# Kernel optimization log

Measured on AMD Instinct MI355X. Metric: run time of the kernel, lower is better.

The kernel has to match this reference:

```python
import jax, jax.numpy as jnp
import numpy as np

B, C, H, W = 4, 256, 64, 64
CR = max(C // 8, 1)  # reduced channels
EPS = 1e-12  # F.normalize eps


def setup_inputs() -> dict:
    key = jax.random.key(0)
    ks = jax.random.split(key, 8)
    s = 1.0 / np.sqrt(C)
    return {
        "x": jax.random.normal(ks[0], (B, C, H, W), dtype=jnp.float32),
        "Wq": jax.random.normal(ks[1], (CR, C), dtype=jnp.float32) * s,
        "bq": jax.random.normal(ks[2], (CR,), dtype=jnp.float32) * s,
        "Wk": jax.random.normal(ks[3], (CR, C), dtype=jnp.float32) * s,
        "bk": jax.random.normal(ks[4], (CR,), dtype=jnp.float32) * s,
        "Wv": jax.random.normal(ks[5], (C, C), dtype=jnp.float32) * s,
        "bv": jax.random.normal(ks[6], (C,), dtype=jnp.float32) * s,
        "gamma": jax.random.normal(ks[7], (1,), dtype=jnp.float32),
    }


def reference(x, Wq, bq, Wk, bk, Wv, bv, gamma):
    b, c, h, w = x.shape
    xf = x.reshape(b, c, h * w)  # [B, C, N]
    # 1x1 convs are per-pixel linear maps
    q = jnp.einsum("rc,bcn->brn", Wq, xf) + bq[None, :, None]  # [B, CR, N]
    k = jnp.einsum("rc,bcn->brn", Wk, xf) + bk[None, :, None]  # [B, CR, N]
    v = jnp.einsum("dc,bcn->bdn", Wv, xf) + bv[None, :, None]  # [B, C, N]
    # attention = bmm(key^T, query): [B, N, N]
    attn = jnp.einsum("brn,brm->bnm", k, q)
    attn = jax.nn.relu(attn)
    # L1 normalize along dim=1 (rows), matching F.normalize(p=1, dim=1)
    denom = jnp.maximum(jnp.sum(jnp.abs(attn), axis=1, keepdims=True), EPS)
    attn = attn / denom
    out = jnp.einsum("bcn,bnm->bcm", v, attn).reshape(b, c, h, w)
    return gamma[0] * out + x
```

## Files before the change

### kernel.cpp

```cpp
#include <hip/hip_runtime.h>
#include <hip/hip_bf16.h>

#define NB 4
#define NC 256
#define NN 4096
#define NCR 32
#define PITCH 72

typedef __attribute__((ext_vector_type(8))) short short8_t;
typedef __attribute__((ext_vector_type(4))) float f32x4;
typedef __attribute__((ext_vector_type(2))) int int2_t;
typedef __attribute__((ext_vector_type(4))) int int4_t;
typedef __attribute__((ext_vector_type(4))) float float4_t;

static __device__ __forceinline__ unsigned short f2bf(float f) {
  unsigned u = __builtin_bit_cast(unsigned, f);
  u += 0x7FFFu + ((u >> 16) & 1u);
  return (unsigned short)(u >> 16);
}

static __device__ __forceinline__ unsigned cvt_pk(float lo, float hi) {
  unsigned r;
  asm("v_cvt_pk_bf16_f32 %0, %1, %2" : "=v"(r) : "v"(lo), "v"(hi));
  return r;
}

static __device__ __forceinline__ void lds_barrier() {
  asm volatile("s_waitcnt lgkmcnt(0)\n\ts_barrier" ::: "memory");
}

__global__ __launch_bounds__(64) void pack_w_kernel(
    const float* __restrict__ Wq, const float* __restrict__ Wk,
    const float* __restrict__ Wv, unsigned short* __restrict__ Wbf)
{
  const int row = blockIdx.x;
  const int t = threadIdx.x;
  const float* src = row < 32 ? Wq + (size_t)row * NC
                   : (row < 64 ? Wk + (size_t)(row - 32) * NC
                               : Wv + (size_t)(row - 64) * NC);
  float4_t v = *(const float4_t*)(src + t * 4);
  int2_t p;
  p[0] = cvt_pk(v[0], v[1]);
  p[1] = cvt_pk(v[2], v[3]);
  *(int2_t*)(Wbf + (size_t)row * NC + t * 4) = p;
}

__global__ __launch_bounds__(256) void xpose_kernel(
    const float* __restrict__ x, unsigned short* __restrict__ xT)
{
  __shared__ float tile[32][65];
  const int bid = blockIdx.x;
  const int mt = bid & 63, kt = (bid >> 6) & 7, b = bid >> 9;
  const int m0 = mt * 64, k0 = kt * 32;
  const int tid = threadIdx.x;

  const float* xb = x + (size_t)b * NC * NN + (size_t)k0 * NN + m0;
#pragma unroll
  for (int p = 0; p < 8; p++) {
    const int r = p * 4 + (tid >> 6);
    tile[r][tid & 63] = xb[(size_t)r * NN + (tid & 63)];
  }
  __syncthreads();

  const int m = tid >> 2, kq = (tid & 3) * 8;
  int4_t o;
#pragma unroll
  for (int j = 0; j < 4; j++)
    o[j] = cvt_pk(tile[kq + 2 * j][m], tile[kq + 2 * j + 1][m]);
  *(int4_t*)(xT + ((size_t)b * NN + m0 + m) * NC + k0 + kq) = o;
}

__global__ __launch_bounds__(256, 2) void qkv_kernel(
    const unsigned short* __restrict__ xT, const unsigned short* __restrict__ Wbf,
    const float* __restrict__ bq, const float* __restrict__ bk,
    const float* __restrict__ bv,
    unsigned short* __restrict__ Qt, unsigned short* __restrict__ Kt,
    unsigned short* __restrict__ Vt)
{
  const int bid = blockIdx.x;
  const int b   = bid >> 7;
  const int m0  = (bid & 127) * 32;
  const int tid = threadIdx.x;
  const int w    = tid >> 6;
  const int lane = tid & 63;
  const int lg   = lane >> 4;
  const int lm   = lane & 15;

  const unsigned short* xrow0 = xT + ((size_t)b * NN + m0 + lm) * NC + lg * 8;
  const unsigned short* xrow1 = xrow0 + 16 * NC;
  const unsigned short* wrow  = Wbf + (size_t)(w * 80 + lm) * NC + lg * 8;

  const f32x4 zero4 = {0.f, 0.f, 0.f, 0.f};
  f32x4 acc[5][2];
#pragma unroll
  for (int df = 0; df < 5; df++)
#pragma unroll
    for (int mf = 0; mf < 2; mf++) acc[df][mf] = zero4;

#pragma unroll
  for (int kc = 0; kc < 8; kc++) {
    const short8_t xf0 = *(const short8_t*)(xrow0 + kc * 32);
    const short8_t xf1 = *(const short8_t*)(xrow1 + kc * 32);
#pragma unroll
    for (int df = 0; df < 5; df++) {
      const short8_t wf = *(const short8_t*)(wrow + (size_t)df * 16 * NC + kc * 32);
      acc[df][0] = __builtin_amdgcn_mfma_f32_16x16x32_bf16(xf0, wf, acc[df][0], 0, 0, 0);
      acc[df][1] = __builtin_amdgcn_mfma_f32_16x16x32_bf16(xf1, wf, acc[df][1], 0, 0, 0);
    }
  }

#pragma unroll
  for (int df = 0; df < 5; df++) {
    const int dbase = w * 80 + df * 16;
    if (dbase < 64) {
      const bool isq = dbase < 32;
      const float bia = isq ? bq[dbase + lm] : bk[dbase - 32 + lm];
      unsigned short* dst = isq ? Qt : Kt;
      const int dcol = (isq ? dbase : dbase - 32) + lm;
#pragma unroll
      for (int mf = 0; mf < 2; mf++)
#pragma unroll
        for (int i = 0; i < 4; i++) {
          const int m = m0 + mf * 16 + lg * 4 + i;
          dst[((size_t)b * NN + m) * NCR + dcol] = f2bf(acc[df][mf][i] + bia);
        }
    } else {
      const int c = dbase - 64 + lm;
      const float bia = bv[c];
#pragma unroll
      for (int mf = 0; mf < 2; mf++) {
        int2_t p;
        p[0] = cvt_pk(acc[df][mf][0] + bia, acc[df][mf][1] + bia);
        p[1] = cvt_pk(acc[df][mf][2] + bia, acc[df][mf][3] + bia);
        *(int2_t*)(Vt + ((size_t)b * NC + c) * NN + m0 + mf * 16 + lg * 4) = p;
      }
    }
  }
}

__global__ __launch_bounds__(256, 2) void attn_kernel(
    const unsigned short* __restrict__ Qt, const unsigned short* __restrict__ Kt,
    const unsigned short* __restrict__ Vt, const float* __restrict__ x,
    const float* __restrict__ gamma, float* __restrict__ out)
{
  __shared__ unsigned short Slds[2][64 * PITCH];
  __shared__ float dlds[4][64];

  const int bid = blockIdx.x;
  const int xcd = bid & 7;
  const int b   = xcd >> 1;
  const int ch  = xcd & 1;
  const int m0  = (bid >> 3) * 64;
  const int tid = threadIdx.x;
  const int w    = tid >> 6;
  const int lane = tid & 63;
  const int lg   = lane >> 4;
  const int lm   = lane & 15;

  const unsigned short* Qb = Qt + (size_t)b * NN * NCR;
  const unsigned short* Kp = Kt + (size_t)b * NN * NCR +
                             (size_t)(w * 16 + lm) * NCR + lg * 8;
  const unsigned short* pV[2];
#pragma unroll
  for (int cf = 0; cf < 2; cf++)
    pV[cf] = Vt + ((size_t)b * NC + ch * 128 + w * 32 + cf * 16 + lm) * NN + lg * 8;

  short8_t qf[4];
#pragma unroll
  for (int mf = 0; mf < 4; mf++)
    qf[mf] = *(const short8_t*)(Qb + (size_t)(m0 + mf * 16 + lm) * NCR + lg * 8);

  const f32x4 zero4 = {0.f, 0.f, 0.f, 0.f};
  f32x4 acc[2][4];
#pragma unroll
  for (int cf = 0; cf < 2; cf++)
#pragma unroll
    for (int mf = 0; mf < 4; mf++) acc[cf][mf] = zero4;
  float dsum[4] = {0.f, 0.f, 0.f, 0.f};

  short8_t kA, kB, vA[2][2], vB[2][2];
  kA = *(const short8_t*)(Kp);
#pragma unroll
  for (int cf = 0; cf < 2; cf++) {
    vA[cf][0] = *(const short8_t*)(pV[cf]);
    vA[cf][1] = *(const short8_t*)(pV[cf] + 32);
  }

  const int swofs = w * 16 + lg * 4;

#define AITER(T, KC, KN, VC, VN, BUF) {                                       \
    const int n1 = (((T) + 1) & 63) * 64;                                     \
        \
    KN = *(const short8_t*)(Kp + (size_t)n1 * NCR);                           \
    _Pragma("unroll") for (int cf = 0; cf < 2; cf++) {                        \
      VN[cf][0] = *(const short8_t*)(pV[cf] + n1);                            \
      VN[cf][1] = *(const short8_t*)(pV[cf] + n1 + 32);                       \
    }                                                                         \
    _Pragma("unroll") for (int mf = 0; mf < 4; mf++) {                        \
      f32x4 s = __builtin_amdgcn_mfma_f32_16x16x32_bf16(KC, qf[mf], zero4, 0, 0, 0); \
      float s0 = fmaxf(s[0], 0.f), s1 = fmaxf(s[1], 0.f);                     \
      float s2 = fmaxf(s[2], 0.f), s3 = fmaxf(s[3], 0.f);                     \
      dsum[mf] += (s0 + s1) + (s2 + s3);                                      \
      int2_t p; p[0] = cvt_pk(s0, s1); p[1] = cvt_pk(s2, s3);                 \
      *(int2_t*)(&Slds[BUF][(mf * 16 + lm) * PITCH + swofs]) = p;             \
    }                                                                         \
    lds_barrier();                                                            \
    __builtin_amdgcn_s_setprio(1);                                            \
    _Pragma("unroll") for (int nch = 0; nch < 2; nch++) {                     \
      short8_t sf[4];                                                         \
      _Pragma("unroll") for (int mf = 0; mf < 4; mf++)                        \
        sf[mf] = *(const short8_t*)(&Slds[BUF][(mf * 16 + lm) * PITCH +       \
                                              nch * 32 + lg * 8]);            \
      _Pragma("unroll") for (int cf = 0; cf < 2; cf++)                        \
        _Pragma("unroll") for (int mf = 0; mf < 4; mf++)                      \
          acc[cf][mf] = __builtin_amdgcn_mfma_f32_16x16x32_bf16(              \
              VC[cf][nch], sf[mf], acc[cf][mf], 0, 0, 0);                     \
    }                                                                         \
    __builtin_amdgcn_s_setprio(0);                                            \
  }

#pragma unroll 1
  for (int t = 0; t < 64; t += 2) {
    AITER(t, kA, kB, vA, vB, 0)
    AITER(t + 1, kB, kA, vB, vA, 1)
  }
#undef AITER

#pragma unroll
  for (int mf = 0; mf < 4; mf++) {
    float v = dsum[mf];
    v += __shfl_xor(v, 16);
    v += __shfl_xor(v, 32);
    if (lane < 16) dlds[w][mf * 16 + lane] = v;
  }
  __syncthreads();

  const float g0 = gamma[0];
  float rden[4];
#pragma unroll
  for (int mf = 0; mf < 4; mf++) {
    const int mloc = mf * 16 + lm;
    float den = dlds[0][mloc] + dlds[1][mloc] + dlds[2][mloc] + dlds[3][mloc];
    den = den > 1e-12f ? den : 1e-12f;
    rden[mf] = 1.0f / den;
  }

  const float* xb = x + (size_t)b * NC * NN;
  float* ob = out + (size_t)b * NC * NN;
#pragma unroll
  for (int cf = 0; cf < 2; cf++) {
#pragma unroll
    for (int i = 0; i < 4; i++) {
      const int c = ch * 128 + w * 32 + cf * 16 + lg * 4 + i;
#pragma unroll
      for (int mf = 0; mf < 4; mf++) {
        const int m = m0 + mf * 16 + lm;
        ob[(size_t)c * NN + m] = g0 * acc[cf][mf][i] * rden[mf] + xb[(size_t)c * NN + m];
      }
    }
  }
}

extern "C" void kernel_launch(void* const* d_in, const int* in_sizes, int n_in,
                              void* d_out, int out_size, void* d_ws, size_t ws_size,
                              hipStream_t stream) {
  const float* x     = (const float*)d_in[0];
  const float* Wq    = (const float*)d_in[1];
  const float* bq    = (const float*)d_in[2];
  const float* Wk    = (const float*)d_in[3];
  const float* bk    = (const float*)d_in[4];
  const float* Wv    = (const float*)d_in[5];
  const float* bv    = (const float*)d_in[6];
  const float* gamma = (const float*)d_in[7];
  float* out = (float*)d_out;

  unsigned short* Wbf = (unsigned short*)d_ws;
  unsigned short* xT  = Wbf + (size_t)320 * NC;
  unsigned short* Qt  = xT + (size_t)NB * NN * NC;
  unsigned short* Kt  = Qt + (size_t)NB * NN * NCR;
  unsigned short* Vt  = Kt + (size_t)NB * NN * NCR;

  hipLaunchKernelGGL(pack_w_kernel, dim3(320), dim3(64), 0, stream,
                     Wq, Wk, Wv, Wbf);
  hipLaunchKernelGGL(xpose_kernel, dim3(2048), dim3(256), 0, stream, x, xT);
  hipLaunchKernelGGL(qkv_kernel, dim3(512), dim3(256), 0, stream,
                     xT, Wbf, bq, bk, bv, Qt, Kt, Vt);
  hipLaunchKernelGGL(attn_kernel, dim3(512), dim3(256), 0, stream,
                     Qt, Kt, Vt, x, gamma, out);
}
```

Before: 102.3 us.

## Fuse x transpose into QKV kernel and software-pipeline attention S computation

Drops the separate transpose kernel. The QKV kernel now reads fp32 x directly, converts it to bf16 and stages it in a swizzled shared-memory tile, double-buffered across four K chunks. This removes a kernel launch and the round trip of the bf16 xT buffer through global memory. In the attention kernel, the score MFMA for the next tile is computed while the current tile's PV accumulation runs, with K prefetched two tiles ahead. This trades extra registers and a restructured barrier schedule for more overlap between the two stages.

```diff
diff --git a/kernel.cpp b/kernel.cpp
--- a/kernel.cpp
+++ b/kernel.cpp
@@ -45,38 +45,15 @@
   *(int2_t*)(Wbf + (size_t)row * NC + t * 4) = p;
 }
 
-__global__ __launch_bounds__(256) void xpose_kernel(
-    const float* __restrict__ x, unsigned short* __restrict__ xT)
-{
-  __shared__ float tile[32][65];
-  const int bid = blockIdx.x;
-  const int mt = bid & 63, kt = (bid >> 6) & 7, b = bid >> 9;
-  const int m0 = mt * 64, k0 = kt * 32;
-  const int tid = threadIdx.x;
-
-  const float* xb = x + (size_t)b * NC * NN + (size_t)k0 * NN + m0;
-#pragma unroll
-  for (int p = 0; p < 8; p++) {
-    const int r = p * 4 + (tid >> 6);
-    tile[r][tid & 63] = xb[(size_t)r * NN + (tid & 63)];
-  }
-  __syncthreads();
-
-  const int m = tid >> 2, kq = (tid & 3) * 8;
-  int4_t o;
-#pragma unroll
-  for (int j = 0; j < 4; j++)
-    o[j] = cvt_pk(tile[kq + 2 * j][m], tile[kq + 2 * j + 1][m]);
-  *(int4_t*)(xT + ((size_t)b * NN + m0 + m) * NC + k0 + kq) = o;
-}
-
 __global__ __launch_bounds__(256, 2) void qkv_kernel(
-    const unsigned short* __restrict__ xT, const unsigned short* __restrict__ Wbf,
+    const float* __restrict__ x, const unsigned short* __restrict__ Wbf,
     const float* __restrict__ bq, const float* __restrict__ bk,
     const float* __restrict__ bv,
     unsigned short* __restrict__ Qt, unsigned short* __restrict__ Kt,
     unsigned short* __restrict__ Vt)
 {
+  __shared__ unsigned short xT[2][32 * 64];
+
   const int bid = blockIdx.x;
   const int b   = bid >> 7;
   const int m0  = (bid & 127) * 32;
@@ -86,9 +63,10 @@
   const int lg   = lane >> 4;
   const int lm   = lane & 15;
 
-  const unsigned short* xrow0 = xT + ((size_t)b * NN + m0 + lm) * NC + lg * 8;
-  const unsigned short* xrow1 = xrow0 + 16 * NC;
-  const unsigned short* wrow  = Wbf + (size_t)(w * 80 + lm) * NC + lg * 8;
+  const int mcol = tid & 31, kg = tid >> 5;
+  const float* xld = x + (size_t)b * NC * NN + (size_t)(kg * 8) * NN + m0 + mcol;
+  const int wofs = mcol * 64 + ((kg ^ (mcol & 7)) << 3);
+  const unsigned short* wrow = Wbf + (size_t)(w * 80 + lm) * NC;
 
   const f32x4 zero4 = {0.f, 0.f, 0.f, 0.f};
   f32x4 acc[5][2];
@@ -97,17 +75,42 @@
 #pragma unroll
     for (int mf = 0; mf < 2; mf++) acc[df][mf] = zero4;
 
-#pragma unroll
-  for (int kc = 0; kc < 8; kc++) {
-    const short8_t xf0 = *(const short8_t*)(xrow0 + kc * 32);
-    const short8_t xf1 = *(const short8_t*)(xrow1 + kc * 32);
-#pragma unroll
-    for (int df = 0; df < 5; df++) {
-      const short8_t wf = *(const short8_t*)(wrow + (size_t)df * 16 * NC + kc * 32);
-      acc[df][0] = __builtin_amdgcn_mfma_f32_16x16x32_bf16(xf0, wf, acc[df][0], 0, 0, 0);
-      acc[df][1] = __builtin_amdgcn_mfma_f32_16x16x32_bf16(xf1, wf, acc[df][1], 0, 0, 0);
-    }
-  }
+  float xg[8], xn[8];
+#pragma unroll
+  for (int j = 0; j < 8; j++) xg[j] = xld[(size_t)j * NN];
+
+#define QCHUNK(C, XC, XN, BUF) {                                              \
+    if ((C) < 3) {                                                            \
+      _Pragma("unroll") for (int j = 0; j < 8; j++)                           \
+        XN[j] = xld[(size_t)(((C) + 1) * 64 + j) * NN];                       \
+    }                                                                         \
+    int4_t xwv;                                                               \
+    xwv[0] = cvt_pk(XC[0], XC[1]); xwv[1] = cvt_pk(XC[2], XC[3]);             \
+    xwv[2] = cvt_pk(XC[4], XC[5]); xwv[3] = cvt_pk(XC[6], XC[7]);             \
+    *(int4_t*)(&xT[BUF][wofs]) = xwv;                                         \
+    __syncthreads();                                                          \
+    _Pragma("unroll") for (int ks = 0; ks < 2; ks++) {                        \
+      short8_t xf[2];                                                         \
+      _Pragma("unroll") for (int mf = 0; mf < 2; mf++) {                      \
+        const int row = mf * 16 + lm;                                         \
+        const int unit = (ks * 4 + lg) ^ (lm & 7);                            \
+        xf[mf] = *(const short8_t*)(&xT[BUF][row * 64 + unit * 8]);           \
+      }                                                                       \
+      _Pragma("unroll") for (int df = 0; df < 5; df++) {                      \
+        const short8_t wf = *(const short8_t*)(wrow + (size_t)df * 16 * NC +  \
+                                               (C) * 64 + ks * 32 + lg * 8);  \
+        _Pragma("unroll") for (int mf = 0; mf < 2; mf++)                      \
+          acc[df][mf] = __builtin_amdgcn_mfma_f32_16x16x32_bf16(              \
+              xf[mf], wf, acc[df][mf], 0, 0, 0);                              \
+      }                                                                       \
+    }                                                                         \
+  }
+
+  QCHUNK(0, xg, xn, 0)
+  QCHUNK(1, xn, xg, 1)
+  QCHUNK(2, xg, xn, 0)
+  QCHUNK(3, xn, xg, 1)
+#undef QCHUNK
 
 #pragma unroll
   for (int df = 0; df < 5; df++) {
@@ -178,53 +181,65 @@
     for (int mf = 0; mf < 4; mf++) acc[cf][mf] = zero4;
   float dsum[4] = {0.f, 0.f, 0.f, 0.f};
 
-  short8_t kA, kB, vA[2][2], vB[2][2];
-  kA = *(const short8_t*)(Kp);
-#pragma unroll
-  for (int cf = 0; cf < 2; cf++) {
-    vA[cf][0] = *(const short8_t*)(pV[cf]);
-    vA[cf][1] = *(const short8_t*)(pV[cf] + 32);
-  }
-
   const int swofs = w * 16 + lg * 4;
 
-#define AITER(T, KC, KN, VC, VN, BUF) {                                       \
-    const int n1 = (((T) + 1) & 63) * 64;                                     \
-        \
-    KN = *(const short8_t*)(Kp + (size_t)n1 * NCR);                           \
-    _Pragma("unroll") for (int cf = 0; cf < 2; cf++) {                        \
-      VN[cf][0] = *(const short8_t*)(pV[cf] + n1);                            \
-      VN[cf][1] = *(const short8_t*)(pV[cf] + n1 + 32);                       \
-    }                                                                         \
+#define SCOMP(KREG, WB) {                                                     \
     _Pragma("unroll") for (int mf = 0; mf < 4; mf++) {                        \
-      f32x4 s = __builtin_amdgcn_mfma_f32_16x16x32_bf16(KC, qf[mf], zero4, 0, 0, 0); \
+      f32x4 s = __builtin_amdgcn_mfma_f32_16x16x32_bf16(KREG, qf[mf], zero4, 0, 0, 0); \
       float s0 = fmaxf(s[0], 0.f), s1 = fmaxf(s[1], 0.f);                     \
       float s2 = fmaxf(s[2], 0.f), s3 = fmaxf(s[3], 0.f);                     \
       dsum[mf] += (s0 + s1) + (s2 + s3);                                      \
       int2_t p; p[0] = cvt_pk(s0, s1); p[1] = cvt_pk(s2, s3);                 \
-      *(int2_t*)(&Slds[BUF][(mf * 16 + lm) * PITCH + swofs]) = p;             \
-    }                                                                         \
-    lds_barrier();                                                            \
+      *(int2_t*)(&Slds[WB][(mf * 16 + lm) * PITCH + swofs]) = p;              \
+    }                                                                         \
+  }
+
+  short8_t kA, kB, vA[2][2], vB[2][2];
+  {
+    const short8_t k0 = *(const short8_t*)(Kp);
+    SCOMP(k0, 0)
+  }
+  kA = *(const short8_t*)(Kp + (size_t)64 * NCR);
+#pragma unroll
+  for (int cf = 0; cf < 2; cf++) {
+    vA[cf][0] = *(const short8_t*)(pV[cf]);
+    vA[cf][1] = *(const short8_t*)(pV[cf] + 32);
+  }
+  lds_barrier();
+
+#define ITER(T, KU, KF, VU, VF, WB, RB, DOS) {                                \
+    const int nk = (((T) + 2) & 63) * 64;                                     \
+    KF = *(const short8_t*)(Kp + (size_t)nk * NCR);                           \
+    const int nv = (((T) + 1) & 63) * 64;                                     \
+    _Pragma("unroll") for (int cf = 0; cf < 2; cf++) {                        \
+      VF[cf][0] = *(const short8_t*)(pV[cf] + nv);                            \
+      VF[cf][1] = *(const short8_t*)(pV[cf] + nv + 32);                       \
+    }                                                                         \
+    if (DOS) { SCOMP(KU, WB) }                                                \
     __builtin_amdgcn_s_setprio(1);                                            \
     _Pragma("unroll") for (int nch = 0; nch < 2; nch++) {                     \
       short8_t sf[4];                                                         \
       _Pragma("unroll") for (int mf = 0; mf < 4; mf++)                        \
-        sf[mf] = *(const short8_t*)(&Slds[BUF][(mf * 16 + lm) * PITCH +       \
-                                              nch * 32 + lg * 8]);            \
+        sf[mf] = *(const short8_t*)(&Slds[RB][(mf * 16 + lm) * PITCH +        \
+                                             nch * 32 + lg * 8]);             \
       _Pragma("unroll") for (int cf = 0; cf < 2; cf++)                        \
         _Pragma("unroll") for (int mf = 0; mf < 4; mf++)                      \
           acc[cf][mf] = __builtin_amdgcn_mfma_f32_16x16x32_bf16(              \
-              VC[cf][nch], sf[mf], acc[cf][mf], 0, 0, 0);                     \
+              VU[cf][nch], sf[mf], acc[cf][mf], 0, 0, 0);                     \
     }                                                                         \
     __builtin_amdgcn_s_setprio(0);                                            \
+    lds_barrier();                                                            \
   }
 
 #pragma unroll 1
-  for (int t = 0; t < 64; t += 2) {
-    AITER(t, kA, kB, vA, vB, 0)
-    AITER(t + 1, kB, kA, vB, vA, 1)
-  }
-#undef AITER
+  for (int t = 0; t < 62; t += 2) {
+    ITER(t, kA, kB, vA, vB, 1, 0, true)
+    ITER(t + 1, kB, kA, vB, vA, 0, 1, true)
+  }
+  ITER(62, kA, kB, vA, vB, 1, 0, true)
+  ITER(63, kB, kA, vB, vA, 0, 1, false)
+#undef ITER
+#undef SCOMP
 
 #pragma unroll
   for (int mf = 0; mf < 4; mf++) {
@@ -275,16 +290,14 @@
   float* out = (float*)d_out;
 
   unsigned short* Wbf = (unsigned short*)d_ws;
-  unsigned short* xT  = Wbf + (size_t)320 * NC;
-  unsigned short* Qt  = xT + (size_t)NB * NN * NC;
+  unsigned short* Qt  = Wbf + (size_t)320 * NC;
   unsigned short* Kt  = Qt + (size_t)NB * NN * NCR;
   unsigned short* Vt  = Kt + (size_t)NB * NN * NCR;
 
   hipLaunchKernelGGL(pack_w_kernel, dim3(320), dim3(64), 0, stream,
                      Wq, Wk, Wv, Wbf);
-  hipLaunchKernelGGL(xpose_kernel, dim3(2048), dim3(256), 0, stream, x, xT);
   hipLaunchKernelGGL(qkv_kernel, dim3(512), dim3(256), 0, stream,
-                     xT, Wbf, bq, bk, bv, Qt, Kt, Vt);
+                     x, Wbf, bq, bk, bv, Qt, Kt, Vt);
   hipLaunchKernelGGL(attn_kernel, dim3(512), dim3(256), 0, stream,
                      Qt, Kt, Vt, x, gamma, out);
 }
```

New measurement: 94.54 us. -7.6%, faster.
